# Optimization experiments

Measured on AMD Instinct MI355X. Metric: run time of the kernel, lower is better.

The kernel has to match this reference:

```python
import jax, jax.numpy as jnp
import numpy as np

B, S, D, H, DFF = 4, 1024, 1024, 16, 4096
MAX_LEN = 1024
DK = D // H
EPS = 1e-5


def _ln(x, g, b):
    m = jnp.mean(x, axis=-1, keepdims=True)
    v = jnp.mean(jnp.square(x - m), axis=-1, keepdims=True)
    return (x - m) / jnp.sqrt(v + EPS) * g + b


def setup_inputs() -> dict:
    key = jax.random.key(0)
    ks = jax.random.split(key, 16)
    s = 0.02
    inp = {
        "x": jax.random.normal(ks[0], (B, S, D), jnp.float32),
        "wq": jax.random.normal(ks[1], (D, D), jnp.float32) * s,
        "bq": jnp.zeros((D,), jnp.float32),
        "wk": jax.random.normal(ks[2], (D, D), jnp.float32) * s,
        "bk": jnp.zeros((D,), jnp.float32),
        "wv": jax.random.normal(ks[3], (D, D), jnp.float32) * s,
        "bv": jnp.zeros((D,), jnp.float32),
        "wo": jax.random.normal(ks[4], (D, D), jnp.float32) * s,
        "bo": jnp.zeros((D,), jnp.float32),
        "rel_table": jax.random.normal(ks[5], (2 * MAX_LEN - 1, H), jnp.float32) * s,
        "ln1_g": jnp.ones((D,), jnp.float32),
        "ln1_b": jnp.zeros((D,), jnp.float32),
        "w1": jax.random.normal(ks[6], (D, DFF), jnp.float32) * s,
        "b1": jnp.zeros((DFF,), jnp.float32),
        "w2": jax.random.normal(ks[7], (DFF, D), jnp.float32) * s,
        "b2": jnp.zeros((D,), jnp.float32),
        "ln2_g": jnp.ones((D,), jnp.float32),
        "ln2_b": jnp.zeros((D,), jnp.float32),
        "mask": jnp.ones((B, 1, 1, S), jnp.int32),
    }
    return inp


def reference(x, wq, bq, wk, bk, wv, bv, wo, bo, rel_table,
              ln1_g, ln1_b, w1, b1, w2, b2, ln2_g, ln2_b, mask):
    # --- multi-head attention with relative position bias (post-LN encoder layer, eval mode) ---
    q = (x @ wq + bq).reshape(B, S, H, DK).transpose(0, 2, 1, 3)  # [B,H,S,dk]
    k = (x @ wk + bk).reshape(B, S, H, DK).transpose(0, 2, 1, 3)
    v = (x @ wv + bv).reshape(B, S, H, DK).transpose(0, 2, 1, 3)

    scores = jnp.einsum('bhqd,bhkd->bhqk', q, k) / jnp.sqrt(jnp.float32(DK))

    # relative position bias: table[(q - k + max_len - 1).clip] -> [1,H,S,S]
    coords = jnp.arange(S)[:, None] - jnp.arange(S)[None, :] + (MAX_LEN - 1)
    coords = jnp.clip(coords, 0, 2 * MAX_LEN - 2)
    bias = rel_table[coords]              # [S,S,H]
    scores = scores + bias.transpose(2, 0, 1)[None]

    scores = jnp.where(mask == 0, jnp.float32(-1e9), scores)
    attn = jax.nn.softmax(scores, axis=-1)
    ctx = jnp.einsum('bhqk,bhkd->bhqd', attn, v)
    ctx = ctx.transpose(0, 2, 1, 3).reshape(B, S, D)
    attn_out = ctx @ wo + bo

    x1 = _ln(x + attn_out, ln1_g, ln1_b)

    ff = jax.nn.relu(x1 @ w1 + b1) @ w2 + b2
    return _ln(x1 + ff, ln2_g, ln2_b)
```

## Files before the change

### kernel.cpp

```cpp
#include <hip/hip_runtime.h>
#include <hip/hip_bf16.h>

typedef __hip_bfloat16 bf16;
typedef __attribute__((ext_vector_type(8))) short short8;
typedef __attribute__((ext_vector_type(4))) float f32x4;

#define LOG2E 1.4426950408889634f

typedef const __attribute__((address_space(1))) void* gptr_t;
typedef __attribute__((address_space(3))) void* sptr_t;

__device__ __forceinline__ void async16(void* lds, const void* g) {
  __builtin_amdgcn_global_load_lds((gptr_t)g, (sptr_t)lds, 16, 0, 0);
}

__device__ __forceinline__ float bf2f(unsigned short u) {
  union { unsigned int i; float f; } c; c.i = ((unsigned int)u) << 16; return c.f;
}


__global__ __launch_bounds__(256) void cast_f2b_kernel(
    const float* __restrict__ src, bf16* __restrict__ dst, int n) {
  int i = (blockIdx.x * 256 + threadIdx.x) * 4;
  if (i >= n) return;
  float4 v = *(const float4*)(src + i);
  bf16 h4[4] = {__float2bfloat16(v.x), __float2bfloat16(v.y),
                __float2bfloat16(v.z), __float2bfloat16(v.w)};
  *(uint2*)((unsigned short*)dst + i) = *(uint2*)h4;
}

__global__ __launch_bounds__(256) void concat_bias(
    const float* __restrict__ bq, const float* __restrict__ bk,
    const float* __restrict__ bv, float* __restrict__ o) {
  int i = blockIdx.x * 256 + threadIdx.x;
  if (i >= 3072) return;
  o[i] = (i < 1024) ? bq[i] : (i < 2048 ? bk[i - 1024] : bv[i - 2048]);
}

__global__ __launch_bounds__(256) void transpose_f2b(
    const float* __restrict__ src, bf16* __restrict__ dst, int K, int N) {
  __shared__ float tl[32][33];
  int n0 = blockIdx.x * 32, k0 = blockIdx.y * 32;
  int tx = threadIdx.x, ty = threadIdx.y;
#pragma unroll
  for (int j = 0; j < 4; ++j)
    tl[ty + j * 8][tx] = src[(size_t)(k0 + ty + j * 8) * N + n0 + tx];
  __syncthreads();
#pragma unroll
  for (int j = 0; j < 4; ++j)
    dst[(size_t)(n0 + ty + j * 8) * K + k0 + tx] =
        __float2bfloat16(tl[tx][ty + j * 8]);
}

__global__ __launch_bounds__(256) void transpose4_f2b(
    const float* __restrict__ s0, const float* __restrict__ s1,
    const float* __restrict__ s2, const float* __restrict__ s3,
    bf16* __restrict__ d0, bf16* __restrict__ d1,
    bf16* __restrict__ d2, bf16* __restrict__ d3) {
  __shared__ float tl[32][33];
  const int z = blockIdx.z;
  const float* src = z == 0 ? s0 : z == 1 ? s1 : z == 2 ? s2 : s3;
  bf16* dst = z == 0 ? d0 : z == 1 ? d1 : z == 2 ? d2 : d3;
  int n0 = blockIdx.x * 32, k0 = blockIdx.y * 32;
  int tx = threadIdx.x, ty = threadIdx.y;
#pragma unroll
  for (int j = 0; j < 4; ++j)
    tl[ty + j * 8][tx] = src[(size_t)(k0 + ty + j * 8) * 1024 + n0 + tx];
  __syncthreads();
#pragma unroll
  for (int j = 0; j < 4; ++j)
    dst[(size_t)(n0 + ty + j * 8) * 1024 + k0 + tx] =
        __float2bfloat16(tl[tx][ty + j * 8]);
}

__global__ __launch_bounds__(256) void build_vt(
    const bf16* __restrict__ qkv, bf16* __restrict__ vt) {
  __shared__ bf16 tl[32][33];
  const int bhz = blockIdx.z, s0 = blockIdx.x * 32, dk0 = blockIdx.y * 32;
  const int b = bhz >> 4, h = bhz & 15;
  const int tx = threadIdx.x, ty = threadIdx.y;
#pragma unroll
  for (int j = 0; j < 4; ++j) {
    int s = s0 + ty + j * 8;
    tl[ty + j * 8][tx] =
        qkv[(size_t)(b * 1024 + s) * 3072 + 2048 + h * 64 + dk0 + tx];
  }
  __syncthreads();
#pragma unroll
  for (int j = 0; j < 4; ++j) {
    int dk = dk0 + ty + j * 8;
    vt[(size_t)(bhz * 64 + dk) * 1024 + s0 + tx] = tl[tx][ty + j * 8];
  }
}


template <int RELU>
__global__ __launch_bounds__(256) void gemm_bt(
    const bf16* __restrict__ A, const bf16* __restrict__ Bt,
    const float* __restrict__ bias, bf16* __restrict__ C, int M, int N, int K) {
  __shared__ bf16 As[128 * 64];
  __shared__ bf16 Bs[128 * 64];
  const int t = threadIdx.x;
  const int w = t >> 6, l = t & 63;
  const int m0 = blockIdx.y * 128, n0 = blockIdx.x * 128;
  const int wr = (w >> 1) * 64, wc = (w & 1) * 64;
  const int srow = l >> 3, scol = l & 7;
  const int lm = l & 15, lq = l >> 4;

  f32x4 acc[4][4];
#pragma unroll
  for (int i = 0; i < 4; ++i)
#pragma unroll
    for (int j = 0; j < 4; ++j) acc[i][j] = (f32x4){0.f, 0.f, 0.f, 0.f};

  for (int k0 = 0; k0 < K; k0 += 64) {
#pragma unroll
    for (int p = 0; p < 4; ++p) {
      int row = p * 32 + w * 8 + srow;
      int gc = scol ^ (row & 7);
      async16(&As[(p * 32 + w * 8) * 64], A + (size_t)(m0 + row) * K + k0 + gc * 8);
      async16(&Bs[(p * 32 + w * 8) * 64], Bt + (size_t)(n0 + row) * K + k0 + gc * 8);
    }
    __syncthreads();
#pragma unroll
    for (int kk = 0; kk < 2; ++kk) {
      short8 af[4], bfr[4];
#pragma unroll
      for (int mi = 0; mi < 4; ++mi) {
        int row = wr + mi * 16 + lm;
        int c = kk * 4 + lq;
        af[mi] = *(const short8*)&As[row * 64 + ((c ^ (row & 7)) << 3)];
      }
#pragma unroll
      for (int ni = 0; ni < 4; ++ni) {
        int row = wc + ni * 16 + lm;
        int c = kk * 4 + lq;
        bfr[ni] = *(const short8*)&Bs[row * 64 + ((c ^ (row & 7)) << 3)];
      }
#pragma unroll
      for (int mi = 0; mi < 4; ++mi)
#pragma unroll
        for (int ni = 0; ni < 4; ++ni)
          acc[mi][ni] = __builtin_amdgcn_mfma_f32_16x16x32_bf16(
              af[mi], bfr[ni], acc[mi][ni], 0, 0, 0);
    }
    __syncthreads();
  }
#pragma unroll
  for (int mi = 0; mi < 4; ++mi)
#pragma unroll
    for (int r = 0; r < 4; ++r) {
      int row = m0 + wr + mi * 16 + lq * 4 + r;
#pragma unroll
      for (int ni = 0; ni < 4; ++ni) {
        int col = n0 + wc + ni * 16 + lm;
        float v = acc[mi][ni][r] + bias[col];
        if (RELU) v = fmaxf(v, 0.f);
        C[(size_t)row * N + col] = __float2bfloat16(v);
      }
    }
}

template <typename OT>
__global__ __launch_bounds__(256) void gemm_bt_splitk(
    const bf16* __restrict__ A, const bf16* __restrict__ Bt,
    OT* __restrict__ P, int M, int N, int lda, int KS) {
  __shared__ bf16 As[128 * 64];
  __shared__ bf16 Bs[128 * 64];
  const int t = threadIdx.x;
  const int w = t >> 6, l = t & 63;
  const int m0 = blockIdx.y * 128, n0 = blockIdx.x * 128;
  const int kstart = blockIdx.z * KS;
  const int wr = (w >> 1) * 64, wc = (w & 1) * 64;
  const int srow = l >> 3, scol = l & 7;
  const int lm = l & 15, lq = l >> 4;

  f32x4 acc[4][4];
#pragma unroll
  for (int i = 0; i < 4; ++i)
#pragma unroll
    for (int j = 0; j < 4; ++j) acc[i][j] = (f32x4){0.f, 0.f, 0.f, 0.f};

  for (int k0 = kstart; k0 < kstart + KS; k0 += 64) {
#pragma unroll
    for (int p = 0; p < 4; ++p) {
      int row = p * 32 + w * 8 + srow;
      int gc = scol ^ (row & 7);
      async16(&As[(p * 32 + w * 8) * 64], A + (size_t)(m0 + row) * lda + k0 + gc * 8);
      async16(&Bs[(p * 32 + w * 8) * 64], Bt + (size_t)(n0 + row) * lda + k0 + gc * 8);
    }
    __syncthreads();
#pragma unroll
    for (int kk = 0; kk < 2; ++kk) {
      short8 af[4], bfr[4];
#pragma unroll
      for (int mi = 0; mi < 4; ++mi) {
        int row = wr + mi * 16 + lm;
        int c = kk * 4 + lq;
        af[mi] = *(const short8*)&As[row * 64 + ((c ^ (row & 7)) << 3)];
      }
#pragma unroll
      for (int ni = 0; ni < 4; ++ni) {
        int row = wc + ni * 16 + lm;
        int c = kk * 4 + lq;
        bfr[ni] = *(const short8*)&Bs[row * 64 + ((c ^ (row & 7)) << 3)];
      }
#pragma unroll
      for (int mi = 0; mi < 4; ++mi)
#pragma unroll
        for (int ni = 0; ni < 4; ++ni)
          acc[mi][ni] = __builtin_amdgcn_mfma_f32_16x16x32_bf16(
              af[mi], bfr[ni], acc[mi][ni], 0, 0, 0);
    }
    __syncthreads();
  }
  OT* Pz = P + (size_t)blockIdx.z * M * N;
#pragma unroll
  for (int mi = 0; mi < 4; ++mi)
#pragma unroll
    for (int r = 0; r < 4; ++r) {
      int row = m0 + wr + mi * 16 + lq * 4 + r;
#pragma unroll
      for (int ni = 0; ni < 4; ++ni) {
        int col = n0 + wc + ni * 16 + lm;
        float v = acc[mi][ni][r];
        if constexpr (sizeof(OT) == 4)
          Pz[(size_t)row * N + col] = v;
        else
          Pz[(size_t)row * N + col] = __float2bfloat16(v);
      }
    }
}


__global__ __launch_bounds__(512, 4) void flash_attn(
    const bf16* __restrict__ qkv, const bf16* __restrict__ vt,
    const float* __restrict__ rel, const int* __restrict__ mask,
    bf16* __restrict__ ctx) {
  __shared__ bf16 Kl[2][64 * 64];
  __shared__ bf16 Vl[2][64 * 64];
  __shared__ bf16 Pl[128 * 64];
  __shared__ float bias_s[2][192];
  __shared__ float mask_s[2][64];

  const int t = threadIdx.x;
  const int w = t >> 6, l = t & 63;
  const int lm = l & 15, lq = l >> 4;
  const int qt = blockIdx.x, bh = blockIdx.y;
  const int b = bh >> 4, h = bh & 15;
  const int q0 = qt * 128;
  const int srow = l >> 3;
  const int gc = (l & 7) ^ srow;
  const int qq = w * 16 + lm;

  auto stage = [&](int d, int k0n) {
    async16(&Kl[d][w * 8 * 64],
            qkv + (size_t)(b * 1024 + k0n + w * 8 + srow) * 3072 + 1024 + h * 64 + gc * 8);
    async16(&Vl[d][w * 8 * 64],
            vt + ((size_t)bh * 64 + w * 8 + srow) * 1024 + k0n + gc * 8);
    if (t < 191) bias_s[d][t] = rel[(q0 - k0n + 960 + t) * 16 + h] * LOG2E;
    if (t < 64) mask_s[d][t] = (mask[b * 1024 + k0n + t] == 0) ? -1.44e9f : 0.f;
  };

#pragma unroll
  for (int p = 0; p < 2; ++p)
    async16(&Pl[(p * 64 + w * 8) * 64],
            qkv + (size_t)(b * 1024 + q0 + p * 64 + w * 8 + srow) * 3072 + h * 64 + gc * 8);
  stage(0, 0);
  __syncthreads();

  short8 qf[2];
#pragma unroll
  for (int kk = 0; kk < 2; ++kk)
    qf[kk] = *(const short8*)&Pl[qq * 64 + (((kk * 4 + lq) ^ (lm & 7)) << 3)];
  __syncthreads();

  float m_st = -1e30f, l_st = 0.f;
  f32x4 acc_o[4];
#pragma unroll
  for (int j = 0; j < 4; ++j) acc_o[j] = (f32x4){0.f, 0.f, 0.f, 0.f};

  const float C0 = 0.125f * LOG2E;

  for (int kt = 0; kt < 16; ++kt) {
    const int d = kt & 1;
    if (kt < 15) stage(d ^ 1, (kt + 1) * 64);

    f32x4 sa[4];
#pragma unroll
    for (int i = 0; i < 4; ++i) sa[i] = (f32x4){0.f, 0.f, 0.f, 0.f};
#pragma unroll
    for (int kk = 0; kk < 2; ++kk) {
      short8 ak[4];
#pragma unroll
      for (int mi = 0; mi < 4; ++mi) {
        int row = mi * 16 + lm;
        ak[mi] = *(const short8*)&Kl[d][row * 64 + (((kk * 4 + lq) ^ (lm & 7)) << 3)];
      }
#pragma unroll
      for (int mi = 0; mi < 4; ++mi)
        sa[mi] = __builtin_amdgcn_mfma_f32_16x16x32_bf16(ak[mi], qf[kk], sa[mi], 0, 0, 0);
    }

    float m4[4][4];
#pragma unroll
    for (int mi = 0; mi < 4; ++mi)
      *(float4*)m4[mi] = *(const float4*)&mask_s[d][mi * 16 + lq * 4];
    float mx = -1e30f;
#pragma unroll
    for (int mi = 0; mi < 4; ++mi)
#pragma unroll
      for (int r = 0; r < 4; ++r) {
        int kl = mi * 16 + lq * 4 + r;
        float v = sa[mi][r] * C0 + (bias_s[d][qq - kl + 63] + m4[mi][r]);
        sa[mi][r] = v;
        mx = fmaxf(mx, v);
      }
    mx = fmaxf(mx, __shfl_xor(mx, 16));
    mx = fmaxf(mx, __shfl_xor(mx, 32));
    float mn = fmaxf(m_st, mx);
    float alpha = __builtin_amdgcn_exp2f(m_st - mn);
    m_st = mn;
    float ls = 0.f;
#pragma unroll
    for (int mi = 0; mi < 4; ++mi)
#pragma unroll
      for (int r = 0; r < 4; ++r) {
        float p = __builtin_amdgcn_exp2f(sa[mi][r] - mn);
        sa[mi][r] = p;
        ls += p;
      }
    ls += __shfl_xor(ls, 16);
    ls += __shfl_xor(ls, 32);
    l_st = l_st * alpha + ls;

#pragma unroll
    for (int mi = 0; mi < 4; ++mi) {
      bf16 h4[4];
#pragma unroll
      for (int r = 0; r < 4; ++r) h4[r] = __float2bfloat16(sa[mi][r]);
      int chunk = mi * 2 + (lq >> 1);
      *(uint2*)&Pl[qq * 64 + ((chunk ^ (lm & 7)) << 3) + ((lq & 1) << 2)] =
          *(uint2*)h4;
    }

#pragma unroll
    for (int r = 0; r < 4; ++r) {
      float a = __shfl(alpha, lq * 4 + r);
#pragma unroll
      for (int ni = 0; ni < 4; ++ni) acc_o[ni][r] *= a;
    }

#pragma unroll
    for (int kk2 = 0; kk2 < 2; ++kk2) {
      short8 pf = *(const short8*)&Pl[qq * 64 + (((kk2 * 4 + lq) ^ (lm & 7)) << 3)];
      short8 vf[4];
#pragma unroll
      for (int ni = 0; ni < 4; ++ni) {
        int rowv = ni * 16 + lm;
        vf[ni] = *(const short8*)&Vl[d][rowv * 64 + (((kk2 * 4 + lq) ^ (lm & 7)) << 3)];
      }
#pragma unroll
      for (int ni = 0; ni < 4; ++ni)
        acc_o[ni] = __builtin_amdgcn_mfma_f32_16x16x32_bf16(pf, vf[ni], acc_o[ni], 0, 0, 0);
    }
    __syncthreads();
  }

  float linv = 1.f / l_st;
#pragma unroll
  for (int r = 0; r < 4; ++r) {
    float il = __shfl(linv, lq * 4 + r);
    int qx = w * 16 + lq * 4 + r;
    size_t rowbase = (size_t)(b * 1024 + q0 + qx) * 1024 + h * 64;
#pragma unroll
    for (int ni = 0; ni < 4; ++ni)
      ctx[rowbase + ni * 16 + lm] = __float2bfloat16(acc_o[ni][r] * il);
  }
}


template <typename PT, int NS>
__global__ __launch_bounds__(256) void ln_resid(
    const float* __restrict__ xin, const PT* __restrict__ part,
    const float* __restrict__ bias,
    const float* __restrict__ gw, const float* __restrict__ bw,
    float* __restrict__ outf, bf16* __restrict__ outb) {
  const int row = blockIdx.x, t = threadIdx.x;
  const size_t base = (size_t)row * 1024 + t * 4;
  float4 xv = *(const float4*)(xin + base);
  float4 bi = *(const float4*)(bias + t * 4);
  float v0 = xv.x + bi.x, v1 = xv.y + bi.y, v2 = xv.z + bi.z, v3 = xv.w + bi.w;
#pragma unroll
  for (int s = 0; s < NS; ++s) {
    const PT* p = part + (size_t)s * 4194304 + base;
    if constexpr (sizeof(PT) == 4) {
      float4 pv = *(const float4*)p;
      v0 += pv.x; v1 += pv.y; v2 += pv.z; v3 += pv.w;
    } else {
      ushort4 pv = *(const ushort4*)p;
      v0 += bf2f(pv.x); v1 += bf2f(pv.y); v2 += bf2f(pv.z); v3 += bf2f(pv.w);
    }
  }
  float s1 = v0 + v1 + v2 + v3;
  float s2 = v0 * v0 + v1 * v1 + v2 * v2 + v3 * v3;
#pragma unroll
  for (int o = 1; o < 64; o <<= 1) {
    s1 += __shfl_xor(s1, o);
    s2 += __shfl_xor(s2, o);
  }
  __shared__ float red[8];
  const int w = t >> 6, l = t & 63;
  if (l == 0) { red[w] = s1; red[4 + w] = s2; }
  __syncthreads();
  float S1 = red[0] + red[1] + red[2] + red[3];
  float S2 = red[4] + red[5] + red[6] + red[7];
  float mean = S1 * (1.f / 1024.f);
  float var = S2 * (1.f / 1024.f) - mean * mean;
  float rstd = rsqrtf(var + 1e-5f);
  float4 gv = *(const float4*)(gw + t * 4);
  float4 bv = *(const float4*)(bw + t * 4);
  float o0 = (v0 - mean) * rstd * gv.x + bv.x;
  float o1 = (v1 - mean) * rstd * gv.y + bv.y;
  float o2 = (v2 - mean) * rstd * gv.z + bv.z;
  float o3 = (v3 - mean) * rstd * gv.w + bv.w;
  if (outf) {
    float4 ov = {o0, o1, o2, o3};
    *(float4*)(outf + base) = ov;
  }
  if (outb) {
    bf16 h4[4] = {__float2bfloat16(o0), __float2bfloat16(o1),
                  __float2bfloat16(o2), __float2bfloat16(o3)};
    *(uint2*)((unsigned short*)outb + base) = *(uint2*)h4;
  }
}


extern "C" void kernel_launch(void* const* d_in, const int* in_sizes, int n_in,
                              void* d_out, int out_size, void* d_ws, size_t ws_size,
                              hipStream_t stream) {
  (void)in_sizes; (void)n_in; (void)out_size; (void)ws_size;
  const float* x   = (const float*)d_in[0];
  const float* wq  = (const float*)d_in[1];
  const float* bq  = (const float*)d_in[2];
  const float* wk  = (const float*)d_in[3];
  const float* bk  = (const float*)d_in[4];
  const float* wv  = (const float*)d_in[5];
  const float* bv  = (const float*)d_in[6];
  const float* wo  = (const float*)d_in[7];
  const float* bo  = (const float*)d_in[8];
  const float* rel = (const float*)d_in[9];
  const float* g1  = (const float*)d_in[10];
  const float* be1 = (const float*)d_in[11];
  const float* w1  = (const float*)d_in[12];
  const float* b1  = (const float*)d_in[13];
  const float* w2  = (const float*)d_in[14];
  const float* b2  = (const float*)d_in[15];
  const float* g2  = (const float*)d_in[16];
  const float* be2 = (const float*)d_in[17];
  const int* mask  = (const int*)d_in[18];
  float* out = (float*)d_out;

  char* ws = (char*)d_ws;
  bf16*  xb      = (bf16*)(ws + 0);
  bf16*  wqkv_t  = (bf16*)(ws + 8388608);
  bf16*  wo_t    = (bf16*)(ws + 14680064);
  bf16*  w1_t    = (bf16*)(ws + 16777216);
  bf16*  ctx_b   = (bf16*)(ws + 25165824);
  bf16*  x1b     = (bf16*)(ws + 33554432);
  bf16*  qkv_b   = (bf16*)(ws + 41943040);
  bf16*  vtb     = (bf16*)(ws + 67108864);
  float* part_wo = (float*)(ws + 41943040);
  bf16*  h1      = (bf16*)(ws + 41943040);
  bf16*  part_ff = (bf16*)(ws + 0);
  bf16*  w2_t    = (bf16*)(ws + 75497472);
  float* x1f     = (float*)(ws + 83886080);
  float* bqkv    = (float*)(ws + 100663296);

  dim3 tb(32, 8);
  cast_f2b_kernel<<<4096, 256, 0, stream>>>(x, xb, 4096 * 1024);
  concat_bias<<<12, 256, 0, stream>>>(bq, bk, bv, bqkv);
  transpose4_f2b<<<dim3(32, 32, 4), tb, 0, stream>>>(
      wq, wk, wv, wo, wqkv_t, wqkv_t + 1024 * 1024, wqkv_t + 2048 * 1024, wo_t);
  transpose_f2b<<<dim3(128, 32), tb, 0, stream>>>(w1, w1_t, 1024, 4096);
  transpose_f2b<<<dim3(32, 128), tb, 0, stream>>>(w2, w2_t, 4096, 1024);

  gemm_bt<0><<<dim3(24, 32), 256, 0, stream>>>(xb, wqkv_t, bqkv, qkv_b, 4096, 3072, 1024);
  build_vt<<<dim3(32, 2, 64), tb, 0, stream>>>(qkv_b, vtb);
  flash_attn<<<dim3(8, 64), 512, 0, stream>>>(qkv_b, vtb, rel, mask, ctx_b);
  gemm_bt_splitk<float><<<dim3(8, 32, 2), 256, 0, stream>>>(
      ctx_b, wo_t, part_wo, 4096, 1024, 1024, 512);
  ln_resid<float, 2><<<4096, 256, 0, stream>>>(x, part_wo, bo, g1, be1, x1f, x1b);
  gemm_bt<1><<<dim3(32, 32), 256, 0, stream>>>(x1b, w1_t, b1, h1, 4096, 4096, 1024);
  gemm_bt_splitk<bf16><<<dim3(8, 32, 4), 256, 0, stream>>>(
      h1, w2_t, part_ff, 4096, 1024, 4096, 1024);
  ln_resid<bf16, 4><<<4096, 256, 0, stream>>>(x1f, part_ff, b2, g2, be2, out, nullptr);
}
```

Measured before the change: 360.3 us.

## Prefetch next GEMM tile during MFMA, merge weight transposes, bf16 Wo partials

The GEMM main loops now load the whole k-tile from LDS into registers, sync, and then issue the async global-to-LDS load for the next tile before running the MFMAs, so global latency overlaps compute within a single LDS buffer. The three weight transpose launches are merged into one kernel with a flat block index. The Wo split-K partials are stored as bf16 instead of fp32, halving that traffic into the layer-norm at some cost in precision. The cost is higher register use for the doubled fragment arrays, which may lower occupancy.

New measurement: 341.4 us. 5.2% less time.

```diff
diff --git a/kernel.cpp b/kernel.cpp
--- a/kernel.cpp
+++ b/kernel.cpp
@@ -37,39 +37,40 @@
   o[i] = (i < 1024) ? bq[i] : (i < 2048 ? bk[i - 1024] : bv[i - 2048]);
 }
 
-__global__ __launch_bounds__(256) void transpose_f2b(
-    const float* __restrict__ src, bf16* __restrict__ dst, int K, int N) {
+__global__ __launch_bounds__(256) void transpose_all(
+    const float* __restrict__ wq, const float* __restrict__ wk,
+    const float* __restrict__ wv, const float* __restrict__ wo,
+    const float* __restrict__ w1, const float* __restrict__ w2,
+    bf16* __restrict__ dqkv, bf16* __restrict__ dwo,
+    bf16* __restrict__ dw1, bf16* __restrict__ dw2) {
   __shared__ float tl[32][33];
-  int n0 = blockIdx.x * 32, k0 = blockIdx.y * 32;
-  int tx = threadIdx.x, ty = threadIdx.y;
+  const int bid = blockIdx.x;
+  const float* s;
+  bf16* d;
+  int NN, KK, n0, k0;
+  if (bid < 4096) {
+    int m = bid >> 10, tile = bid & 1023;
+    s = m == 0 ? wq : m == 1 ? wk : m == 2 ? wv : wo;
+    d = m < 3 ? dqkv + (size_t)m * 1024 * 1024 : dwo;
+    NN = 1024; KK = 1024;
+    n0 = (tile & 31) * 32; k0 = (tile >> 5) * 32;
+  } else if (bid < 8192) {
+    int tile = bid - 4096;
+    s = w1; d = dw1; NN = 4096; KK = 1024;
+    n0 = (tile & 127) * 32; k0 = (tile >> 7) * 32;
+  } else {
+    int tile = bid - 8192;
+    s = w2; d = dw2; NN = 1024; KK = 4096;
+    n0 = (tile & 31) * 32; k0 = (tile >> 5) * 32;
+  }
+  const int tx = threadIdx.x & 31, ty = threadIdx.x >> 5;
 #pragma unroll
   for (int j = 0; j < 4; ++j)
-    tl[ty + j * 8][tx] = src[(size_t)(k0 + ty + j * 8) * N + n0 + tx];
+    tl[ty + j * 8][tx] = s[(size_t)(k0 + ty + j * 8) * NN + n0 + tx];
   __syncthreads();
 #pragma unroll
   for (int j = 0; j < 4; ++j)
-    dst[(size_t)(n0 + ty + j * 8) * K + k0 + tx] =
-        __float2bfloat16(tl[tx][ty + j * 8]);
-}
-
-__global__ __launch_bounds__(256) void transpose4_f2b(
-    const float* __restrict__ s0, const float* __restrict__ s1,
-    const float* __restrict__ s2, const float* __restrict__ s3,
-    bf16* __restrict__ d0, bf16* __restrict__ d1,
-    bf16* __restrict__ d2, bf16* __restrict__ d3) {
-  __shared__ float tl[32][33];
-  const int z = blockIdx.z;
-  const float* src = z == 0 ? s0 : z == 1 ? s1 : z == 2 ? s2 : s3;
-  bf16* dst = z == 0 ? d0 : z == 1 ? d1 : z == 2 ? d2 : d3;
-  int n0 = blockIdx.x * 32, k0 = blockIdx.y * 32;
-  int tx = threadIdx.x, ty = threadIdx.y;
-#pragma unroll
-  for (int j = 0; j < 4; ++j)
-    tl[ty + j * 8][tx] = src[(size_t)(k0 + ty + j * 8) * 1024 + n0 + tx];
-  __syncthreads();
-#pragma unroll
-  for (int j = 0; j < 4; ++j)
-    dst[(size_t)(n0 + ty + j * 8) * 1024 + k0 + tx] =
+    d[(size_t)(n0 + ty + j * 8) * KK + k0 + tx] =
         __float2bfloat16(tl[tx][ty + j * 8]);
 }
 
@@ -113,7 +114,7 @@
 #pragma unroll
     for (int j = 0; j < 4; ++j) acc[i][j] = (f32x4){0.f, 0.f, 0.f, 0.f};
 
-  for (int k0 = 0; k0 < K; k0 += 64) {
+  auto stage = [&](int k0) {
 #pragma unroll
     for (int p = 0; p < 4; ++p) {
       int row = p * 32 + w * 8 + srow;
@@ -121,30 +122,32 @@
       async16(&As[(p * 32 + w * 8) * 64], A + (size_t)(m0 + row) * K + k0 + gc * 8);
       async16(&Bs[(p * 32 + w * 8) * 64], Bt + (size_t)(n0 + row) * K + k0 + gc * 8);
     }
+  };
+
+  stage(0);
+  const int niter = K >> 6;
+  for (int it = 0; it < niter; ++it) {
     __syncthreads();
-#pragma unroll
-    for (int kk = 0; kk < 2; ++kk) {
-      short8 af[4], bfr[4];
+    short8 af[2][4], bfr[2][4];
+#pragma unroll
+    for (int kk = 0; kk < 2; ++kk)
 #pragma unroll
       for (int mi = 0; mi < 4; ++mi) {
-        int row = wr + mi * 16 + lm;
-        int c = kk * 4 + lq;
-        af[mi] = *(const short8*)&As[row * 64 + ((c ^ (row & 7)) << 3)];
-      }
-#pragma unroll
-      for (int ni = 0; ni < 4; ++ni) {
-        int row = wc + ni * 16 + lm;
-        int c = kk * 4 + lq;
-        bfr[ni] = *(const short8*)&Bs[row * 64 + ((c ^ (row & 7)) << 3)];
-      }
+        int rowa = wr + mi * 16 + lm;
+        af[kk][mi] = *(const short8*)&As[rowa * 64 + (((kk * 4 + lq) ^ (rowa & 7)) << 3)];
+        int rowb = wc + mi * 16 + lm;
+        bfr[kk][mi] = *(const short8*)&Bs[rowb * 64 + (((kk * 4 + lq) ^ (rowb & 7)) << 3)];
+      }
+    __syncthreads();
+    if (it + 1 < niter) stage((it + 1) << 6);
+#pragma unroll
+    for (int kk = 0; kk < 2; ++kk)
 #pragma unroll
       for (int mi = 0; mi < 4; ++mi)
 #pragma unroll
         for (int ni = 0; ni < 4; ++ni)
           acc[mi][ni] = __builtin_amdgcn_mfma_f32_16x16x32_bf16(
-              af[mi], bfr[ni], acc[mi][ni], 0, 0, 0);
-    }
-    __syncthreads();
+              af[kk][mi], bfr[kk][ni], acc[mi][ni], 0, 0, 0);
   }
 #pragma unroll
   for (int mi = 0; mi < 4; ++mi)
@@ -181,7 +184,7 @@
 #pragma unroll
     for (int j = 0; j < 4; ++j) acc[i][j] = (f32x4){0.f, 0.f, 0.f, 0.f};
 
-  for (int k0 = kstart; k0 < kstart + KS; k0 += 64) {
+  auto stage = [&](int k0) {
 #pragma unroll
     for (int p = 0; p < 4; ++p) {
       int row = p * 32 + w * 8 + srow;
@@ -189,30 +192,32 @@
       async16(&As[(p * 32 + w * 8) * 64], A + (size_t)(m0 + row) * lda + k0 + gc * 8);
       async16(&Bs[(p * 32 + w * 8) * 64], Bt + (size_t)(n0 + row) * lda + k0 + gc * 8);
     }
+  };
+
+  stage(kstart);
+  const int niter = KS >> 6;
+  for (int it = 0; it < niter; ++it) {
     __syncthreads();
-#pragma unroll
-    for (int kk = 0; kk < 2; ++kk) {
-      short8 af[4], bfr[4];
+    short8 af[2][4], bfr[2][4];
+#pragma unroll
+    for (int kk = 0; kk < 2; ++kk)
 #pragma unroll
       for (int mi = 0; mi < 4; ++mi) {
-        int row = wr + mi * 16 + lm;
-        int c = kk * 4 + lq;
-        af[mi] = *(const short8*)&As[row * 64 + ((c ^ (row & 7)) << 3)];
-      }
-#pragma unroll
-      for (int ni = 0; ni < 4; ++ni) {
-        int row = wc + ni * 16 + lm;
-        int c = kk * 4 + lq;
-        bfr[ni] = *(const short8*)&Bs[row * 64 + ((c ^ (row & 7)) << 3)];
-      }
+        int rowa = wr + mi * 16 + lm;
+        af[kk][mi] = *(const short8*)&As[rowa * 64 + (((kk * 4 + lq) ^ (rowa & 7)) << 3)];
+        int rowb = wc + mi * 16 + lm;
+        bfr[kk][mi] = *(const short8*)&Bs[rowb * 64 + (((kk * 4 + lq) ^ (rowb & 7)) << 3)];
+      }
+    __syncthreads();
+    if (it + 1 < niter) stage(kstart + ((it + 1) << 6));
+#pragma unroll
+    for (int kk = 0; kk < 2; ++kk)
 #pragma unroll
       for (int mi = 0; mi < 4; ++mi)
 #pragma unroll
         for (int ni = 0; ni < 4; ++ni)
           acc[mi][ni] = __builtin_amdgcn_mfma_f32_16x16x32_bf16(
-              af[mi], bfr[ni], acc[mi][ni], 0, 0, 0);
-    }
-    __syncthreads();
+              af[kk][mi], bfr[kk][ni], acc[mi][ni], 0, 0, 0);
   }
   OT* Pz = P + (size_t)blockIdx.z * M * N;
 #pragma unroll
@@ -470,7 +475,7 @@
   bf16*  x1b     = (bf16*)(ws + 33554432);
   bf16*  qkv_b   = (bf16*)(ws + 41943040);
   bf16*  vtb     = (bf16*)(ws + 67108864);
-  float* part_wo = (float*)(ws + 41943040);
+  bf16*  part_wo = (bf16*)(ws + 41943040);
   bf16*  h1      = (bf16*)(ws + 41943040);
   bf16*  part_ff = (bf16*)(ws + 0);
   bf16*  w2_t    = (bf16*)(ws + 75497472);
@@ -480,17 +485,15 @@
   dim3 tb(32, 8);
   cast_f2b_kernel<<<4096, 256, 0, stream>>>(x, xb, 4096 * 1024);
   concat_bias<<<12, 256, 0, stream>>>(bq, bk, bv, bqkv);
-  transpose4_f2b<<<dim3(32, 32, 4), tb, 0, stream>>>(
-      wq, wk, wv, wo, wqkv_t, wqkv_t + 1024 * 1024, wqkv_t + 2048 * 1024, wo_t);
-  transpose_f2b<<<dim3(128, 32), tb, 0, stream>>>(w1, w1_t, 1024, 4096);
-  transpose_f2b<<<dim3(32, 128), tb, 0, stream>>>(w2, w2_t, 4096, 1024);
+  transpose_all<<<12288, 256, 0, stream>>>(
+      wq, wk, wv, wo, w1, w2, wqkv_t, wo_t, w1_t, w2_t);
 
   gemm_bt<0><<<dim3(24, 32), 256, 0, stream>>>(xb, wqkv_t, bqkv, qkv_b, 4096, 3072, 1024);
   build_vt<<<dim3(32, 2, 64), tb, 0, stream>>>(qkv_b, vtb);
   flash_attn<<<dim3(8, 64), 512, 0, stream>>>(qkv_b, vtb, rel, mask, ctx_b);
-  gemm_bt_splitk<float><<<dim3(8, 32, 2), 256, 0, stream>>>(
+  gemm_bt_splitk<bf16><<<dim3(8, 32, 2), 256, 0, stream>>>(
       ctx_b, wo_t, part_wo, 4096, 1024, 1024, 512);
-  ln_resid<float, 2><<<4096, 256, 0, stream>>>(x, part_wo, bo, g1, be1, x1f, x1b);
+  ln_resid<bf16, 2><<<4096, 256, 0, stream>>>(x, part_wo, bo, g1, be1, x1f, x1b);
   gemm_bt<1><<<dim3(32, 32), 256, 0, stream>>>(x1b, w1_t, b1, h1, 4096, 4096, 1024);
   gemm_bt_splitk<bf16><<<dim3(8, 32, 4), 256, 0, stream>>>(
       h1, w2_t, part_ff, 4096, 1024, 4096, 1024);
```
